# Kernel tuning notes

Measured on AMD Instinct MI355X. Metric: run time of the kernel, lower is better.

## Reference

```python
import jax, jax.numpy as jnp
import numpy as np


def get_grid_index(init_grid_size, map_size):
    # nearest-neighbor 'interpolation' of flat indices, matching F.interpolate(mode='nearest')
    H_init, W_init = init_grid_size
    H, W = map_size
    # torch nearest: src index = floor(dst * scale), scale = src/dst
    rows = jnp.floor(jnp.arange(H_init) * (H / H_init)).astype(jnp.int32)
    cols = jnp.floor(jnp.arange(W_init) * (W / W_init)).astype(jnp.int32)
    idx = rows[:, None] * W + cols[None, :]
    return idx.reshape(-1)  # [N_init]


def _map2token(feature_map, idx_token, N, H_init, W_init):
    B, C, H, W = feature_map.shape
    N_init = H_init * W_init
    idx_hw = get_grid_index((H_init, W_init), (H, W))  # [N_init]
    # gather per-grid feature values: fm_flat[b, idx_hw] -> [B, N_init, C]
    fm = feature_map.transpose(0, 2, 3, 1).reshape(B, H * W, C)
    src = fm[:, idx_hw, :]  # [B, N_init, C]
    # scatter-add into tokens with counts
    def scatter_b(src_b, idx_b):
        num = jnp.zeros((N, C), src_b.dtype).at[idx_b].add(src_b)
        cnt = jnp.zeros((N,), src_b.dtype).at[idx_b].add(1.0)
        return num / (cnt + 1e-6)[:, None]
    return jax.vmap(scatter_b)(src, idx_token)  # [B, N, C]


def _token2map(x, idx_token, H, W, H_init, W_init):
    B, N, C = x.shape
    N_init = H_init * W_init
    idx_hw = get_grid_index((H_init, W_init), (H, W))  # [N_init]
    # each initial grid point contributes token x[b, idx_token[b,i]] to map cell idx_hw[i]
    def scatter_b(x_b, idx_tok_b):
        src = x_b[idx_tok_b]  # [N_init, C]
        num = jnp.zeros((H * W, C), x_b.dtype).at[idx_hw].add(src)
        cnt = jnp.zeros((H * W,), x_b.dtype).at[idx_hw].add(1.0)
        return num / (cnt + 1e-6)[:, None]
    out = jax.vmap(scatter_b)(x, idx_token)  # [B, H*W, C]
    return out.reshape(B, H, W, C).transpose(0, 3, 1, 2)


def setup_inputs() -> dict:
    key = jax.random.key(0)
    k1, k2, k3 = jax.random.split(key, 3)
    B, C, H, W = 8, 256, 56, 56
    N = 784
    H_init = W_init = 56
    N_init = H_init * W_init
    feature_map = jax.random.normal(k1, (B, C, H, W), dtype=jnp.float32)
    x = jax.random.normal(k2, (B, N, C), dtype=jnp.float32)
    idx_token = jax.random.randint(k3, (B, N_init), 0, N)
    return {"feature_map": feature_map, "x": x, "idx_token": idx_token,
            "token_num": N, "map_H": H, "map_W": W, "init_H": H_init, "init_W": W_init}


def reference(feature_map, x, idx_token, token_num, map_H, map_W, init_H, init_W):
    tokens = _map2token(feature_map, idx_token, token_num, init_H, init_W)
    fmap = _token2map(x, idx_token, map_H, map_W, init_H, init_W)
    return tokens, fmap
```

## Files before the change

### kernel.cpp

```cpp
#include <hip/hip_runtime.h>

#define BATCH 8
#define CCH   256
#define HWSZ  3136
#define NTOK  784
#define NINIT 3136

#define TOK_BLOCKS  (BATCH * NTOK)
#define FMAP_TI     (HWSZ / 64)
#define FMAP_TC     (CCH / 64)
#define FMAP_BLOCKS (BATCH * FMAP_TI * FMAP_TC)

__global__ __launch_bounds__(256) void fused_kernel(
    const float* __restrict__ fm,
    const float* __restrict__ x,
    const int*   __restrict__ idx,
    float*       __restrict__ tokens,
    float*       __restrict__ fmap)
{
    __shared__ __align__(16) char smem[64 * 65 * 4 + 256];
    const int bid = blockIdx.x;
    const int tid = threadIdx.x;

    if (bid < TOK_BLOCKS) {
        const int b = bid & 7;
        const int n = bid >> 3;

        int* list   = (int*)smem;
        int* countp = (int*)(smem + NINIT * 4);
        if (tid == 0) *countp = 0;
        __syncthreads();

        const int4* idx4 = (const int4*)(idx + b * NINIT);
        for (int i = tid; i < NINIT / 4; i += 256) {
            int4 v = idx4[i];
            if (v.x == n) list[atomicAdd(countp, 1)] = 4 * i + 0;
            if (v.y == n) list[atomicAdd(countp, 1)] = 4 * i + 1;
            if (v.z == n) list[atomicAdd(countp, 1)] = 4 * i + 2;
            if (v.w == n) list[atomicAdd(countp, 1)] = 4 * i + 3;
        }
        __syncthreads();

        const int m = *countp;
        const int c = tid;
        const float* fmb = fm + ((size_t)b * CCH + c) * HWSZ;
        float s = 0.0f;
        for (int k = 0; k < m; ++k) s += fmb[list[k]];

        tokens[((size_t)b * NTOK + n) * CCH + c] = s / ((float)m + 1e-6f);
    } else {
        int t = bid - TOK_BLOCKS;
        const int b  = t & 7;  t >>= 3;
        const int ct = t & 3;  t >>= 2;
        const int it = t;
        const int i0 = it * 64;
        const int c0 = ct * 64;

        float (*tile)[65] = (float (*)[65])smem;
        int* ns = (int*)(smem + 64 * 65 * 4);

        const int lane = tid & 63;
        const int rr   = tid >> 6;

        if (tid < 64) ns[tid] = idx[b * NINIT + i0 + tid];
        __syncthreads();

        const int q  = tid & 15;
        const int r0 = tid >> 4;
        for (int p = 0; p < 4; ++p) {
            const int r = r0 + p * 16;
            const float4 v = *(const float4*)&x[((size_t)b * NTOK + ns[r]) * CCH + c0 + q * 4];
            tile[r][q * 4 + 0] = v.x;
            tile[r][q * 4 + 1] = v.y;
            tile[r][q * 4 + 2] = v.z;
            tile[r][q * 4 + 3] = v.w;
        }
        __syncthreads();

        const float inv = 1.0f / (1.0f + 1e-6f);
        float* outb = fmap + (size_t)b * CCH * HWSZ;
        for (int cc = rr; cc < 64; cc += 4) {
            outb[(size_t)(c0 + cc) * HWSZ + i0 + lane] = tile[lane][cc] * inv;
        }
    }
}

extern "C" void kernel_launch(void* const* d_in, const int* in_sizes, int n_in,
                              void* d_out, int out_size, void* d_ws, size_t ws_size,
                              hipStream_t stream) {
    const float* fm  = (const float*)d_in[0];
    const float* x   = (const float*)d_in[1];
    const int*   idx = (const int*)d_in[2];

    float* tokens = (float*)d_out;
    float* fmap   = (float*)d_out + (size_t)BATCH * NTOK * CCH;

    fused_kernel<<<TOK_BLOCKS + FMAP_BLOCKS, 256, 0, stream>>>(fm, x, idx, tokens, fmap);
}
```

Before: 121.1 us.

## Transpose feature map and prebuild token index lists for coalesced token gathers

Splits the work into a prep kernel and a tokens kernel. The prep kernel transposes the feature map to channel-last in workspace, computes the fmap output, and builds per-token lists of source positions with global atomics. The tokens kernel then reads precomputed lists and gathers contiguous channel rows. This removes the per-block full scan of the index array and the strided channel-major gathers. In exchange it adds a memset, an extra launch, the workspace transpose traffic, and a cap of 64 entries per token list.

```diff
diff --git a/kernel.cpp b/kernel.cpp
--- a/kernel.cpp
+++ b/kernel.cpp
@@ -5,60 +5,71 @@
 #define HWSZ  3136
 #define NTOK  784
 #define NINIT 3136
+#define MAXM  64
 
-#define TOK_BLOCKS  (BATCH * NTOK)
-#define FMAP_TI     (HWSZ / 64)
-#define FMAP_TC     (CCH / 64)
-#define FMAP_BLOCKS (BATCH * FMAP_TI * FMAP_TC)
+#define FMT_OFF   0
+#define CNT_OFF   25690112
+#define SLOT_OFF  25715200
 
-__global__ __launch_bounds__(256) void fused_kernel(
+#define TRANS_BLOCKS (BATCH * 49 * 4)
+#define FMAP_BLOCKS  (BATCH * 49 * 4)
+#define CSR_BLOCKS   BATCH
+#define K1_BLOCKS    (TRANS_BLOCKS + FMAP_BLOCKS + CSR_BLOCKS)
+#define TOK_BLOCKS   (BATCH * NTOK)
+
+__global__ __launch_bounds__(256) void prep_kernel(
     const float* __restrict__ fm,
     const float* __restrict__ x,
     const int*   __restrict__ idx,
-    float*       __restrict__ tokens,
-    float*       __restrict__ fmap)
+    float*       __restrict__ fmap,
+    float*       __restrict__ fmT,
+    int*         __restrict__ cnt,
+    int*         __restrict__ slot)
 {
-    __shared__ __align__(16) char smem[64 * 65 * 4 + 256];
+    __shared__ __align__(16) float tile[64][65];
     const int bid = blockIdx.x;
     const int tid = threadIdx.x;
 
-    if (bid < TOK_BLOCKS) {
-        const int b = bid & 7;
-        const int n = bid >> 3;
+    if (bid < TRANS_BLOCKS) {
+        const int b  = bid & 7;
+        int t = bid >> 3;
+        const int ct = t & 3;
+        const int it = t >> 2;
+        const int c0 = ct * 64;
+        const int i0 = it * 64;
 
-        int* list   = (int*)smem;
-        int* countp = (int*)(smem + NINIT * 4);
-        if (tid == 0) *countp = 0;
-        __syncthreads();
+        const int q  = tid & 15;
+        const int r0 = tid >> 4;
 
-        const int4* idx4 = (const int4*)(idx + b * NINIT);
-        for (int i = tid; i < NINIT / 4; i += 256) {
-            int4 v = idx4[i];
-            if (v.x == n) list[atomicAdd(countp, 1)] = 4 * i + 0;
-            if (v.y == n) list[atomicAdd(countp, 1)] = 4 * i + 1;
-            if (v.z == n) list[atomicAdd(countp, 1)] = 4 * i + 2;
-            if (v.w == n) list[atomicAdd(countp, 1)] = 4 * i + 3;
+        #pragma unroll
+        for (int p = 0; p < 4; ++p) {
+            const int r = r0 + p * 16;
+            const float4 v = *(const float4*)&fm[((size_t)(b * CCH + c0 + r)) * HWSZ + i0 + q * 4];
+            tile[r][q * 4 + 0] = v.x;
+            tile[r][q * 4 + 1] = v.y;
+            tile[r][q * 4 + 2] = v.z;
+            tile[r][q * 4 + 3] = v.w;
         }
         __syncthreads();
-
-        const int m = *countp;
-        const int c = tid;
-        const float* fmb = fm + ((size_t)b * CCH + c) * HWSZ;
-        float s = 0.0f;
-        for (int k = 0; k < m; ++k) s += fmb[list[k]];
-
-        tokens[((size_t)b * NTOK + n) * CCH + c] = s / ((float)m + 1e-6f);
-    } else {
-        int t = bid - TOK_BLOCKS;
+        #pragma unroll
+        for (int p = 0; p < 4; ++p) {
+            const int i = r0 + p * 16;
+            float4 w;
+            w.x = tile[q * 4 + 0][i];
+            w.y = tile[q * 4 + 1][i];
+            w.z = tile[q * 4 + 2][i];
+            w.w = tile[q * 4 + 3][i];
+            *(float4*)&fmT[((size_t)(b * HWSZ + i0 + i)) * CCH + c0 + q * 4] = w;
+        }
+    } else if (bid < TRANS_BLOCKS + FMAP_BLOCKS) {
+        int t = bid - TRANS_BLOCKS;
         const int b  = t & 7;  t >>= 3;
         const int ct = t & 3;  t >>= 2;
         const int it = t;
         const int i0 = it * 64;
         const int c0 = ct * 64;
 
-        float (*tile)[65] = (float (*)[65])smem;
-        int* ns = (int*)(smem + 64 * 65 * 4);
-
+        __shared__ int ns[64];
         const int lane = tid & 63;
         const int rr   = tid >> 6;
 
@@ -67,6 +78,7 @@
 
         const int q  = tid & 15;
         const int r0 = tid >> 4;
+        #pragma unroll
         for (int p = 0; p < 4; ++p) {
             const int r = r0 + p * 16;
             const float4 v = *(const float4*)&x[((size_t)b * NTOK + ns[r]) * CCH + c0 + q * 4];
@@ -79,10 +91,42 @@
 
         const float inv = 1.0f / (1.0f + 1e-6f);
         float* outb = fmap + (size_t)b * CCH * HWSZ;
+        #pragma unroll
         for (int cc = rr; cc < 64; cc += 4) {
             outb[(size_t)(c0 + cc) * HWSZ + i0 + lane] = tile[lane][cc] * inv;
         }
+    } else {
+        const int b = bid - (TRANS_BLOCKS + FMAP_BLOCKS);
+        for (int i = tid; i < NINIT; i += 256) {
+            const int n = idx[b * NINIT + i];
+            const int p = atomicAdd(&cnt[b * NTOK + n], 1);
+            if (p < MAXM) slot[(b * NTOK + n) * MAXM + p] = i;
+        }
     }
+}
+
+__global__ __launch_bounds__(256) void tokens_kernel(
+    const float* __restrict__ fmT,
+    const int*   __restrict__ cnt,
+    const int*   __restrict__ slot,
+    float*       __restrict__ tokens)
+{
+    const int bid = blockIdx.x;
+    const int tid = threadIdx.x;
+    const int b = bid & 7;
+    const int n = bid >> 3;
+
+    __shared__ int list[MAXM];
+    const int mraw = cnt[b * NTOK + n];
+    const int m = mraw < MAXM ? mraw : MAXM;
+    if (tid < m) list[tid] = slot[(b * NTOK + n) * MAXM + tid];
+    __syncthreads();
+
+    const float* base = fmT + (size_t)b * HWSZ * CCH + tid;
+    float s = 0.0f;
+    for (int k = 0; k < m; ++k) s += base[(size_t)list[k] * CCH];
+
+    tokens[((size_t)b * NTOK + n) * CCH + tid] = s / ((float)mraw + 1e-6f);
 }
 
 extern "C" void kernel_launch(void* const* d_in, const int* in_sizes, int n_in,
@@ -95,5 +139,12 @@
     float* tokens = (float*)d_out;
     float* fmap   = (float*)d_out + (size_t)BATCH * NTOK * CCH;
 
-    fused_kernel<<<TOK_BLOCKS + FMAP_BLOCKS, 256, 0, stream>>>(fm, x, idx, tokens, fmap);
+    char* ws   = (char*)d_ws;
+    float* fmT = (float*)(ws + FMT_OFF);
+    int*   cnt = (int*)(ws + CNT_OFF);
+    int*   slot= (int*)(ws + SLOT_OFF);
+
+    hipMemsetAsync(cnt, 0, BATCH * NTOK * sizeof(int), stream);
+    prep_kernel<<<K1_BLOCKS, 256, 0, stream>>>(fm, x, idx, fmap, fmT, cnt, slot);
+    tokens_kernel<<<TOK_BLOCKS, 256, 0, stream>>>(fmT, cnt, slot, tokens);
 }
```

After: 115.8 us. 4.4% less time.

## Replace per-token gather with precomputed counts and coalesced atomic scatter-add

Applied to the files above, without the earlier changes.

The map-to-token path used to launch one block per token. Each block scanned all index entries to build a member list, then did strided gathers from the feature map. It now runs in three steps: a small kernel counts members per token and stores reciprocals in workspace, a memset zeroes the token output, and tiled blocks read feature-map tiles coalesced, transpose them through shared memory, and scatter pre-scaled values with float atomics. This removes the redundant full index scan per token and the uncoalesced reads. In exchange it adds two extra launches, atomic contention, and a nondeterministic summation order.

```diff
diff --git a/kernel.cpp b/kernel.cpp
--- a/kernel.cpp
+++ b/kernel.cpp
@@ -6,58 +6,84 @@
 #define NTOK  784
 #define NINIT 3136
 
-#define TOK_BLOCKS  (BATCH * NTOK)
-#define FMAP_TI     (HWSZ / 64)
-#define FMAP_TC     (CCH / 64)
-#define FMAP_BLOCKS (BATCH * FMAP_TI * FMAP_TC)
+#define SCAT_BLOCKS (BATCH * 49 * 4)
+#define FMAP_BLOCKS (BATCH * 49 * 4)
+#define K_BLOCKS    (SCAT_BLOCKS + FMAP_BLOCKS)
+
+__global__ __launch_bounds__(256) void cnt_kernel(
+    const int* __restrict__ idx,
+    float*     __restrict__ inv)
+{
+    __shared__ int cnt[NTOK];
+    const int b = blockIdx.x;
+    for (int n = threadIdx.x; n < NTOK; n += 256) cnt[n] = 0;
+    __syncthreads();
+    for (int i = threadIdx.x; i < NINIT; i += 256)
+        atomicAdd(&cnt[idx[b * NINIT + i]], 1);
+    __syncthreads();
+    for (int n = threadIdx.x; n < NTOK; n += 256)
+        inv[b * NTOK + n] = 1.0f / ((float)cnt[n] + 1e-6f);
+}
 
 __global__ __launch_bounds__(256) void fused_kernel(
     const float* __restrict__ fm,
     const float* __restrict__ x,
     const int*   __restrict__ idx,
+    const float* __restrict__ inv,
     float*       __restrict__ tokens,
     float*       __restrict__ fmap)
 {
-    __shared__ __align__(16) char smem[64 * 65 * 4 + 256];
+    __shared__ __align__(16) float tile[64][65];
+    __shared__ int   ns[64];
+    __shared__ float invv[64];
+
     const int bid = blockIdx.x;
     const int tid = threadIdx.x;
+    const int q  = tid & 15;
+    const int r0 = tid >> 4;
 
-    if (bid < TOK_BLOCKS) {
-        const int b = bid & 7;
-        const int n = bid >> 3;
+    if (bid < SCAT_BLOCKS) {
+        const int b  = bid & 7;
+        int t = bid >> 3;
+        const int ct = t & 3;
+        const int it = t >> 2;
+        const int c0 = ct * 64;
+        const int i0 = it * 64;
 
-        int* list   = (int*)smem;
-        int* countp = (int*)(smem + NINIT * 4);
-        if (tid == 0) *countp = 0;
-        __syncthreads();
-
-        const int4* idx4 = (const int4*)(idx + b * NINIT);
-        for (int i = tid; i < NINIT / 4; i += 256) {
-            int4 v = idx4[i];
-            if (v.x == n) list[atomicAdd(countp, 1)] = 4 * i + 0;
-            if (v.y == n) list[atomicAdd(countp, 1)] = 4 * i + 1;
-            if (v.z == n) list[atomicAdd(countp, 1)] = 4 * i + 2;
-            if (v.w == n) list[atomicAdd(countp, 1)] = 4 * i + 3;
+        if (tid < 64) {
+            const int n = idx[b * NINIT + i0 + tid];
+            ns[tid]   = n;
+            invv[tid] = inv[b * NTOK + n];
+        }
+        #pragma unroll
+        for (int p = 0; p < 4; ++p) {
+            const int r = r0 + p * 16;
+            const float4 v = *(const float4*)&fm[((size_t)(b * CCH + c0 + r)) * HWSZ + i0 + q * 4];
+            tile[r][q * 4 + 0] = v.x;
+            tile[r][q * 4 + 1] = v.y;
+            tile[r][q * 4 + 2] = v.z;
+            tile[r][q * 4 + 3] = v.w;
         }
         __syncthreads();
 
-        const int m = *countp;
-        const int c = tid;
-        const float* fmb = fm + ((size_t)b * CCH + c) * HWSZ;
-        float s = 0.0f;
-        for (int k = 0; k < m; ++k) s += fmb[list[k]];
-
-        tokens[((size_t)b * NTOK + n) * CCH + c] = s / ((float)m + 1e-6f);
+        #pragma unroll
+        for (int p = 0; p < 4; ++p) {
+            const int i = r0 + p * 16;
+            const int n = ns[i];
+            const float s = invv[i];
+            float* dst = &tokens[((size_t)b * NTOK + n) * CCH + c0 + q * 4];
+            atomicAdd(dst + 0, tile[q * 4 + 0][i] * s);
+            atomicAdd(dst + 1, tile[q * 4 + 1][i] * s);
+            atomicAdd(dst + 2, tile[q * 4 + 2][i] * s);
+            atomicAdd(dst + 3, tile[q * 4 + 3][i] * s);
+        }
     } else {
-        int t = bid - TOK_BLOCKS;
+        int t = bid - SCAT_BLOCKS;
         const int b  = t & 7;  t >>= 3;
         const int ct = t & 3;  t >>= 2;
         const int it = t;
         const int i0 = it * 64;
         const int c0 = ct * 64;
-
-        float (*tile)[65] = (float (*)[65])smem;
-        int* ns = (int*)(smem + 64 * 65 * 4);
 
         const int lane = tid & 63;
         const int rr   = tid >> 6;
@@ -65,8 +91,7 @@
         if (tid < 64) ns[tid] = idx[b * NINIT + i0 + tid];
         __syncthreads();
 
-        const int q  = tid & 15;
-        const int r0 = tid >> 4;
+        #pragma unroll
         for (int p = 0; p < 4; ++p) {
             const int r = r0 + p * 16;
             const float4 v = *(const float4*)&x[((size_t)b * NTOK + ns[r]) * CCH + c0 + q * 4];
@@ -77,10 +102,11 @@
         }
         __syncthreads();
 
-        const float inv = 1.0f / (1.0f + 1e-6f);
+        const float invc = 1.0f / (1.0f + 1e-6f);
         float* outb = fmap + (size_t)b * CCH * HWSZ;
+        #pragma unroll
         for (int cc = rr; cc < 64; cc += 4) {
-            outb[(size_t)(c0 + cc) * HWSZ + i0 + lane] = tile[lane][cc] * inv;
+            outb[(size_t)(c0 + cc) * HWSZ + i0 + lane] = tile[lane][cc] * invc;
         }
     }
 }
@@ -94,6 +120,9 @@
 
     float* tokens = (float*)d_out;
     float* fmap   = (float*)d_out + (size_t)BATCH * NTOK * CCH;
+    float* inv    = (float*)d_ws;
 
-    fused_kernel<<<TOK_BLOCKS + FMAP_BLOCKS, 256, 0, stream>>>(fm, x, idx, tokens, fmap);
+    hipMemsetAsync(tokens, 0, (size_t)BATCH * NTOK * CCH * sizeof(float), stream);
+    cnt_kernel<<<BATCH, 256, 0, stream>>>(idx, inv);
+    fused_kernel<<<K_BLOCKS, 256, 0, stream>>>(fm, x, idx, inv, tokens, fmap);
 }
```

Measured after the change: 184.8 us. +52.6%, slower.

## Restructure map2token as per-channel-plane scatter-add into shared memory accumulators

Applied to the files above, without the earlier changes.

The token path no longer gives each block one token that scans all indices and gathers strided feature-map values. Each block now owns a batch and a group of four channels. It loads contiguous channel planes into LDS and scatter-adds them into per-token shared accumulators with LDS atomics, and per-token counts come from a shared histogram. This replaces the N×NINIT index scans and uncoalesced gathers with coalesced plane reads, at the cost of LDS atomic contention, fewer token blocks (512), and higher shared memory use that may lower occupancy. The fmap path only gains unroll pragmas.

```diff
diff --git a/kernel.cpp b/kernel.cpp
--- a/kernel.cpp
+++ b/kernel.cpp
@@ -6,10 +6,11 @@
 #define NTOK  784
 #define NINIT 3136
 
-#define TOK_BLOCKS  (BATCH * NTOK)
-#define FMAP_TI     (HWSZ / 64)
-#define FMAP_TC     (CCH / 64)
-#define FMAP_BLOCKS (BATCH * FMAP_TI * FMAP_TC)
+#define TOK_BLOCKS  (BATCH * 64)
+#define FMAP_BLOCKS (BATCH * 49 * 4)
+#define GRID        (TOK_BLOCKS + FMAP_BLOCKS)
+
+#define SMEM_BYTES 34496
 
 __global__ __launch_bounds__(256) void fused_kernel(
     const float* __restrict__ fm,
@@ -18,37 +19,54 @@
     float*       __restrict__ tokens,
     float*       __restrict__ fmap)
 {
-    __shared__ __align__(16) char smem[64 * 65 * 4 + 256];
+    __shared__ __align__(16) char smem[SMEM_BYTES];
     const int bid = blockIdx.x;
     const int tid = threadIdx.x;
 
     if (bid < TOK_BLOCKS) {
-        const int b = bid & 7;
-        const int n = bid >> 3;
+        float* plane = (float*)smem;
+        float* acc   = (float*)(smem + 25088);
+        int*   cnt_s = (int*)(smem + 25088 + 6272);
 
-        int* list   = (int*)smem;
-        int* countp = (int*)(smem + NINIT * 4);
-        if (tid == 0) *countp = 0;
+        const int b  = bid & 7;
+        const int c0 = (bid >> 3) * 4;
+        const int* ib = idx + b * NINIT;
+
+        for (int n = tid; n < NTOK; n += 256) cnt_s[n] = 0;
         __syncthreads();
+        for (int i = tid; i < NINIT; i += 256) atomicAdd(&cnt_s[ib[i]], 1);
 
-        const int4* idx4 = (const int4*)(idx + b * NINIT);
-        for (int i = tid; i < NINIT / 4; i += 256) {
-            int4 v = idx4[i];
-            if (v.x == n) list[atomicAdd(countp, 1)] = 4 * i + 0;
-            if (v.y == n) list[atomicAdd(countp, 1)] = 4 * i + 1;
-            if (v.z == n) list[atomicAdd(countp, 1)] = 4 * i + 2;
-            if (v.w == n) list[atomicAdd(countp, 1)] = 4 * i + 3;
+        #pragma unroll
+        for (int pair = 0; pair < 2; ++pair) {
+            const int c = c0 + pair * 2;
+            for (int n = tid; n < NTOK; n += 256) {
+                *(float2*)&acc[n * 2] = make_float2(0.f, 0.f);
+            }
+            const float4* src = (const float4*)&fm[(size_t)(b * CCH + c) * HWSZ];
+            float4* pl4 = (float4*)plane;
+            for (int v = tid; v < 2 * (HWSZ / 4); v += 256) pl4[v] = src[v];
+            __syncthreads();
+
+            for (int i = tid; i < NINIT; i += 256) {
+                const int n = ib[i];
+                atomicAdd(&acc[n * 2 + 0], plane[i]);
+                atomicAdd(&acc[n * 2 + 1], plane[HWSZ + i]);
+            }
+            __syncthreads();
+
+            for (int n = tid; n < NTOK; n += 256) {
+                const float s = 1.0f / ((float)cnt_s[n] + 1e-6f);
+                float2 w;
+                w.x = acc[n * 2 + 0] * s;
+                w.y = acc[n * 2 + 1] * s;
+                *(float2*)&tokens[((size_t)(b * NTOK + n)) * CCH + c] = w;
+            }
+            __syncthreads();
         }
-        __syncthreads();
+    } else {
+        float (*tile)[65] = (float (*)[65])smem;
+        int* ns = (int*)(smem + 64 * 65 * 4);
 
-        const int m = *countp;
-        const int c = tid;
-        const float* fmb = fm + ((size_t)b * CCH + c) * HWSZ;
-        float s = 0.0f;
-        for (int k = 0; k < m; ++k) s += fmb[list[k]];
-
-        tokens[((size_t)b * NTOK + n) * CCH + c] = s / ((float)m + 1e-6f);
-    } else {
         int t = bid - TOK_BLOCKS;
         const int b  = t & 7;  t >>= 3;
         const int ct = t & 3;  t >>= 2;
@@ -56,20 +74,18 @@
         const int i0 = it * 64;
         const int c0 = ct * 64;
 
-        float (*tile)[65] = (float (*)[65])smem;
-        int* ns = (int*)(smem + 64 * 65 * 4);
-
         const int lane = tid & 63;
         const int rr   = tid >> 6;
+        const int q    = tid & 15;
+        const int r0   = tid >> 4;
 
         if (tid < 64) ns[tid] = idx[b * NINIT + i0 + tid];
         __syncthreads();
 
-        const int q  = tid & 15;
-        const int r0 = tid >> 4;
+        #pragma unroll
         for (int p = 0; p < 4; ++p) {
             const int r = r0 + p * 16;
-            const float4 v = *(const float4*)&x[((size_t)b * NTOK + ns[r]) * CCH + c0 + q * 4];
+            const float4 v = *(const float4*)&x[((size_t)(b * NTOK + ns[r])) * CCH + c0 + q * 4];
             tile[r][q * 4 + 0] = v.x;
             tile[r][q * 4 + 1] = v.y;
             tile[r][q * 4 + 2] = v.z;
@@ -77,10 +93,11 @@
         }
         __syncthreads();
 
-        const float inv = 1.0f / (1.0f + 1e-6f);
+        const float invc = 1.0f / (1.0f + 1e-6f);
         float* outb = fmap + (size_t)b * CCH * HWSZ;
+        #pragma unroll
         for (int cc = rr; cc < 64; cc += 4) {
-            outb[(size_t)(c0 + cc) * HWSZ + i0 + lane] = tile[lane][cc] * inv;
+            outb[(size_t)(c0 + cc) * HWSZ + i0 + lane] = tile[lane][cc] * invc;
         }
     }
 }
@@ -95,5 +112,5 @@
     float* tokens = (float*)d_out;
     float* fmap   = (float*)d_out + (size_t)BATCH * NTOK * CCH;
 
-    fused_kernel<<<TOK_BLOCKS + FMAP_BLOCKS, 256, 0, stream>>>(fm, x, idx, tokens, fmap);
+    fused_kernel<<<GRID, 256, 0, stream>>>(fm, x, idx, tokens, fmap);
 }
```

Result: slower. 133.3 us (+10.1%).
